# Optimization experiments

Hardware: AMD Instinct MI355X
Metric: run time of the kernel (lower is better)

The kernel has to match this reference:

```python
import jax, jax.numpy as jnp
import numpy as np

N_NODES = 500_000
N_Q = 500_000
H = 8       # heads
MH = 8      # m // heads


def setup_inputs() -> dict:
    key = jax.random.key(0)
    ks = jax.random.split(key, 6)
    q_phi = jax.random.normal(ks[0], (N_Q, H, MH), dtype=jnp.float32)
    phi_k_pos = jax.random.normal(ks[1], (H, MH, N_NODES), dtype=jnp.float32)
    phi_k_neg = jax.random.normal(ks[2], (H, MH, N_NODES), dtype=jnp.float32)
    # degrees are nonnegative counts accumulated in build(); simulate with scaled uniforms
    deg_pos = jax.random.uniform(ks[3], (N_NODES, H), dtype=jnp.float32) * 32.0
    deg_neg = jax.random.uniform(ks[4], (N_NODES, H), dtype=jnp.float32) * 32.0
    k_indices = jax.random.randint(ks[5], (N_Q,), 0, N_NODES)
    return {
        "q_phi": q_phi,
        "phi_k_pos": phi_k_pos,
        "phi_k_neg": phi_k_neg,
        "deg_pos": deg_pos,
        "deg_neg": deg_neg,
        "k_indices": k_indices,
    }


def reference(q_phi, phi_k_pos, phi_k_neg, deg_pos, deg_neg, k_indices):
    # gather cached per-node random-feature sums: [h, mh, Nq] -> [Nq, h, mh]
    pk_pos = jnp.transpose(phi_k_pos[:, :, k_indices], (2, 0, 1))
    pk_neg = jnp.transpose(phi_k_neg[:, :, k_indices], (2, 0, 1))
    # per-head dot product over the feature chunk
    num_pos = jnp.sum(q_phi * pk_pos, axis=-1)  # [Nq, h]
    num_neg = jnp.sum(q_phi * pk_neg, axis=-1)  # [Nq, h]
    # degree-normalize with clamp_min(1)
    den_pos = jnp.maximum(deg_pos[k_indices], 1.0)  # [Nq, h]
    den_neg = jnp.maximum(deg_neg[k_indices], 1.0)
    return (num_pos / den_pos, num_neg / den_neg)
```

## Files before the change

kernel.cpp:

```cpp
#include <hip/hip_runtime.h>
#include <hip/hip_bf16.h>

constexpr int N_NODES = 500000;
constexpr int N_Q     = 500000;
constexpr int H       = 8;
constexpr int FEAT    = 64;
constexpr int TILES   = (N_NODES + 63) / 64;

__global__ __launch_bounds__(256) void transpose_pk(
    const float* __restrict__ pk_pos,
    const float* __restrict__ pk_neg,
    float* __restrict__ dst)
{
    __shared__ float lds[64 * 65];
    const int t  = threadIdx.x;
    const int n0 = blockIdx.x * 64;
    const float* src = blockIdx.y ? pk_neg : pk_pos;
    float* d = dst + (size_t)blockIdx.y * (size_t)N_NODES * FEAT;

    const int nrem = N_NODES - n0;

    {
        const int n4 = (t & 15) * 4;
        const int fb = t >> 4;
        for (int it = 0; it < 4; ++it) {
            const int f = fb + it * 16;
            float4 v = make_float4(0.f, 0.f, 0.f, 0.f);
            const float* s = src + (size_t)f * N_NODES + n0 + n4;
            if (n4 + 3 < nrem) {
                v = *(const float4*)s;
            } else if (n4 < nrem) {
                v.x = s[0];
                if (n4 + 1 < nrem) v.y = s[1];
                if (n4 + 2 < nrem) v.z = s[2];
            }
            float* l = &lds[f * 65 + n4];
            l[0] = v.x; l[1] = v.y; l[2] = v.z; l[3] = v.w;
        }
    }
    __syncthreads();

    {
        const int f4 = (t & 15) * 4;
        const int nb = t >> 4;
        for (int it = 0; it < 4; ++it) {
            const int n = nb + it * 16;
            if (n < nrem) {
                float4 v;
                v.x = lds[(f4 + 0) * 65 + n];
                v.y = lds[(f4 + 1) * 65 + n];
                v.z = lds[(f4 + 2) * 65 + n];
                v.w = lds[(f4 + 3) * 65 + n];
                *(float4*)(d + (size_t)(n0 + n) * FEAT + f4) = v;
            }
        }
    }
}

__global__ __launch_bounds__(256) void iskde_main2(
    const float* __restrict__ q_phi,
    const float* __restrict__ pk_t,
    const float* __restrict__ deg_pos,
    const float* __restrict__ deg_neg,
    const int*   __restrict__ k_idx,
    float*       __restrict__ out)
{
    const int i = blockIdx.x * 256 + threadIdx.x;
    const int q = i >> 3;
    const int h = i & 7;

    const int j = k_idx[q];

    const float4* qp = (const float4*)(q_phi + (size_t)q * FEAT + h * 8);
    const float4* pp = (const float4*)(pk_t + (size_t)j * FEAT + h * 8);
    const float4* pn = (const float4*)(pk_t + ((size_t)N_NODES + (size_t)j) * FEAT + h * 8);

    const float4 a0 = qp[0], a1 = qp[1];
    const float4 b0 = pp[0], b1 = pp[1];
    const float4 c0 = pn[0], c1 = pn[1];

    float sp = a0.x*b0.x + a0.y*b0.y + a0.z*b0.z + a0.w*b0.w
             + a1.x*b1.x + a1.y*b1.y + a1.z*b1.z + a1.w*b1.w;
    float sn = a0.x*c0.x + a0.y*c0.y + a0.z*c0.z + a0.w*c0.w
             + a1.x*c1.x + a1.y*c1.y + a1.z*c1.z + a1.w*c1.w;

    const float dp = fmaxf(deg_pos[(size_t)j * H + h], 1.0f);
    const float dn = fmaxf(deg_neg[(size_t)j * H + h], 1.0f);

    __builtin_nontemporal_store(sp / dp, &out[i]);
    __builtin_nontemporal_store(sn / dn, &out[(size_t)N_Q * H + i]);
}

__global__ __launch_bounds__(256, 4) void iskde_gather_kernel(
    const float* __restrict__ q_phi,
    const float* __restrict__ pk_pos,
    const float* __restrict__ pk_neg,
    const float* __restrict__ deg_pos,
    const float* __restrict__ deg_neg,
    const int*   __restrict__ k_idx,
    float*       __restrict__ out)
{
    const int wave_in_blk = threadIdx.x >> 6;
    const int lane        = threadIdx.x & 63;
    const int q           = blockIdx.x * 4 + wave_in_blk;
    if (q >= N_Q) return;

    const int j = k_idx[q];
    const float qv = q_phi[(size_t)q * FEAT + lane];
    const size_t col = (size_t)lane * (size_t)N_NODES + (size_t)j;
    const float pv = pk_pos[col];
    const float nv = pk_neg[col];

    float sp = qv * pv;
    float sn = qv * nv;
    sp += __shfl_xor(sp, 1, 64);
    sn += __shfl_xor(sn, 1, 64);
    sp += __shfl_xor(sp, 2, 64);
    sn += __shfl_xor(sn, 2, 64);
    sp += __shfl_xor(sp, 4, 64);
    sn += __shfl_xor(sn, 4, 64);

    if ((lane & 7) == 0) {
        const int h = lane >> 3;
        const float dp = fmaxf(deg_pos[(size_t)j * H + h], 1.0f);
        const float dn = fmaxf(deg_neg[(size_t)j * H + h], 1.0f);
        const size_t o = (size_t)q * H + h;
        out[o]                   = sp / dp;
        out[(size_t)N_Q * H + o] = sn / dn;
    }
}

extern "C" void kernel_launch(void* const* d_in, const int* in_sizes, int n_in,
                              void* d_out, int out_size, void* d_ws, size_t ws_size,
                              hipStream_t stream) {
    const float* q_phi   = (const float*)d_in[0];
    const float* pk_pos  = (const float*)d_in[1];
    const float* pk_neg  = (const float*)d_in[2];
    const float* deg_pos = (const float*)d_in[3];
    const float* deg_neg = (const float*)d_in[4];
    const int*   k_idx   = (const int*)d_in[5];
    float*       out     = (float*)d_out;

    const size_t need = (size_t)2 * N_NODES * FEAT * sizeof(float);

    if (ws_size >= need) {
        float* pk_t = (float*)d_ws;
        dim3 tgrid(TILES, 2);
        transpose_pk<<<tgrid, 256, 0, stream>>>(pk_pos, pk_neg, pk_t);

        const int blocks = (N_Q * H) / 256;
        iskde_main2<<<blocks, 256, 0, stream>>>(
            q_phi, pk_t, deg_pos, deg_neg, k_idx, out);
    } else {
        const int blocks = (N_Q + 3) / 4;
        iskde_gather_kernel<<<blocks, 256, 0, stream>>>(
            q_phi, pk_pos, pk_neg, deg_pos, deg_neg, k_idx, out);
    }
}
```

Measured before the change: 452.4 us.

## Bin queries by node tile and compute from LDS-staged feature tiles

Replaces the full transpose of both feature tables into workspace with a counting sort of queries by 64-node bin (histogram, scan, atomic scatter). Each block then loads one 64-node tile of pos/neg features into LDS and answers all queries that map to it. This avoids writing and rereading a 256MB transposed copy. The cost is five small launches, a single-block scan, atomics, and scattered reads of q_phi and output writes in bin order.

```diff
diff --git a/kernel.cpp b/kernel.cpp
--- a/kernel.cpp
+++ b/kernel.cpp
@@ -1,94 +1,159 @@
 #include <hip/hip_runtime.h>
-#include <hip/hip_bf16.h>
 
 constexpr int N_NODES = 500000;
 constexpr int N_Q     = 500000;
 constexpr int H       = 8;
 constexpr int FEAT    = 64;
-constexpr int TILES   = (N_NODES + 63) / 64;
-
-__global__ __launch_bounds__(256) void transpose_pk(
+
+constexpr int TBIN   = 64;
+constexpr int SHIFT  = 6;
+constexpr int NB     = (N_NODES + TBIN - 1) / TBIN;
+constexpr int NB_PAD = 8192;
+constexpr int TP     = TBIN + 1;
+
+__global__ __launch_bounds__(256) void zero_hist(int* __restrict__ hist)
+{
+    const int i = blockIdx.x * 256 + threadIdx.x;
+    if (i < NB_PAD) hist[i] = 0;
+}
+
+__global__ __launch_bounds__(256) void hist_kernel(const int* __restrict__ k_idx,
+                                                   int* __restrict__ hist)
+{
+    int i = blockIdx.x * blockDim.x + threadIdx.x;
+    const int stride = gridDim.x * blockDim.x;
+    for (; i < N_Q; i += stride)
+        atomicAdd(&hist[k_idx[i] >> SHIFT], 1);
+}
+
+__global__ __launch_bounds__(1024) void scan_kernel(const int* __restrict__ hist,
+                                                    int* __restrict__ offsets,
+                                                    int* __restrict__ cursor)
+{
+    __shared__ int sums[1024];
+    const int tid  = threadIdx.x;
+    const int base = tid * 8;
+
+    int loc[8];
+    int run = 0;
+#pragma unroll
+    for (int k = 0; k < 8; ++k) {
+        loc[k] = run;
+        const int idx = base + k;
+        run += (idx < NB) ? hist[idx] : 0;
+    }
+    sums[tid] = run;
+    __syncthreads();
+
+    const int own = run;
+    for (int d = 1; d < 1024; d <<= 1) {
+        const int add = (tid >= d) ? sums[tid - d] : 0;
+        __syncthreads();
+        sums[tid] += add;
+        __syncthreads();
+    }
+    const int excl = sums[tid] - own;
+
+#pragma unroll
+    for (int k = 0; k < 8; ++k) {
+        const int idx = base + k;
+        if (idx <= NB) {
+            const int v = excl + loc[k];
+            offsets[idx] = v;
+            cursor[idx]  = v;
+        }
+    }
+}
+
+__global__ __launch_bounds__(256) void scatter_kernel(const int* __restrict__ k_idx,
+                                                      int* __restrict__ cursor,
+                                                      unsigned* __restrict__ vals)
+{
+    int i = blockIdx.x * blockDim.x + threadIdx.x;
+    const int stride = gridDim.x * blockDim.x;
+    for (; i < N_Q; i += stride) {
+        const int j = k_idx[i];
+        const int b = j >> SHIFT;
+        const int p = atomicAdd(&cursor[b], 1);
+        vals[p] = ((unsigned)i << SHIFT) | (unsigned)(j & (TBIN - 1));
+    }
+}
+
+__global__ __launch_bounds__(256, 4) void iskde_binned(
+    const float* __restrict__ q_phi,
     const float* __restrict__ pk_pos,
     const float* __restrict__ pk_neg,
-    float* __restrict__ dst)
-{
-    __shared__ float lds[64 * 65];
-    const int t  = threadIdx.x;
-    const int n0 = blockIdx.x * 64;
-    const float* src = blockIdx.y ? pk_neg : pk_pos;
-    float* d = dst + (size_t)blockIdx.y * (size_t)N_NODES * FEAT;
-
-    const int nrem = N_NODES - n0;
-
-    {
-        const int n4 = (t & 15) * 4;
-        const int fb = t >> 4;
+    const float* __restrict__ deg_pos,
+    const float* __restrict__ deg_neg,
+    const unsigned* __restrict__ vals,
+    const int* __restrict__ offsets,
+    float* __restrict__ out)
+{
+    __shared__ float lds[2][FEAT][TP];
+
+    const int tid  = threadIdx.x;
+    const int b    = blockIdx.x;
+    const int n0   = b * TBIN;
+    const int nrem = min(TBIN, N_NODES - n0);
+
+#pragma unroll
+    for (int s = 0; s < 2; ++s) {
+        const float* __restrict__ src = s ? pk_neg : pk_pos;
+#pragma unroll
         for (int it = 0; it < 4; ++it) {
-            const int f = fb + it * 16;
+            const int g  = it * 256 + tid;
+            const int f  = g >> 4;
+            const int n4 = (g & 15) * 4;
+            const float* p = src + (size_t)f * N_NODES + n0 + n4;
             float4 v = make_float4(0.f, 0.f, 0.f, 0.f);
-            const float* s = src + (size_t)f * N_NODES + n0 + n4;
             if (n4 + 3 < nrem) {
-                v = *(const float4*)s;
-            } else if (n4 < nrem) {
-                v.x = s[0];
-                if (n4 + 1 < nrem) v.y = s[1];
-                if (n4 + 2 < nrem) v.z = s[2];
+                v = *(const float4*)p;
+            } else {
+                if (n4 + 0 < nrem) v.x = p[0];
+                if (n4 + 1 < nrem) v.y = p[1];
+                if (n4 + 2 < nrem) v.z = p[2];
+                if (n4 + 3 < nrem) v.w = p[3];
             }
-            float* l = &lds[f * 65 + n4];
+            float* l = &lds[s][f][n4];
             l[0] = v.x; l[1] = v.y; l[2] = v.z; l[3] = v.w;
         }
     }
     __syncthreads();
 
-    {
-        const int f4 = (t & 15) * 4;
-        const int nb = t >> 4;
-        for (int it = 0; it < 4; ++it) {
-            const int n = nb + it * 16;
-            if (n < nrem) {
-                float4 v;
-                v.x = lds[(f4 + 0) * 65 + n];
-                v.y = lds[(f4 + 1) * 65 + n];
-                v.z = lds[(f4 + 2) * 65 + n];
-                v.w = lds[(f4 + 3) * 65 + n];
-                *(float4*)(d + (size_t)(n0 + n) * FEAT + f4) = v;
-            }
+    const int start = offsets[b];
+    const int count = offsets[b + 1] - start;
+    const int h    = tid & 7;
+    const int slot = tid >> 3;
+
+    for (int it0 = 0; it0 < count; it0 += 32) {
+        const int qi    = it0 + slot;
+        const bool valid = qi < count;
+        unsigned v = 0;
+        if (valid) v = vals[start + qi];
+        const int q  = (int)(v >> SHIFT);
+        const int dj = (int)(v & (TBIN - 1));
+
+        const float4* qp = (const float4*)(q_phi + (size_t)q * FEAT + h * 8);
+        const float4 a0 = qp[0];
+        const float4 a1 = qp[1];
+
+        const float* lp = &lds[0][h * 8][dj];
+        const float* ln = &lds[1][h * 8][dj];
+        float sp = a0.x * lp[0]      + a0.y * lp[TP]     + a0.z * lp[2 * TP] + a0.w * lp[3 * TP]
+                 + a1.x * lp[4 * TP] + a1.y * lp[5 * TP] + a1.z * lp[6 * TP] + a1.w * lp[7 * TP];
+        float sn = a0.x * ln[0]      + a0.y * ln[TP]     + a0.z * ln[2 * TP] + a0.w * ln[3 * TP]
+                 + a1.x * ln[4 * TP] + a1.y * ln[5 * TP] + a1.z * ln[6 * TP] + a1.w * ln[7 * TP];
+
+        const int j = n0 + dj;
+        const float dp = fmaxf(deg_pos[(size_t)j * H + h], 1.0f);
+        const float dn = fmaxf(deg_neg[(size_t)j * H + h], 1.0f);
+
+        if (valid) {
+            const size_t o = (size_t)q * H + h;
+            __builtin_nontemporal_store(sp / dp, &out[o]);
+            __builtin_nontemporal_store(sn / dn, &out[(size_t)N_Q * H + o]);
         }
     }
-}
-
-__global__ __launch_bounds__(256) void iskde_main2(
-    const float* __restrict__ q_phi,
-    const float* __restrict__ pk_t,
-    const float* __restrict__ deg_pos,
-    const float* __restrict__ deg_neg,
-    const int*   __restrict__ k_idx,
-    float*       __restrict__ out)
-{
-    const int i = blockIdx.x * 256 + threadIdx.x;
-    const int q = i >> 3;
-    const int h = i & 7;
-
-    const int j = k_idx[q];
-
-    const float4* qp = (const float4*)(q_phi + (size_t)q * FEAT + h * 8);
-    const float4* pp = (const float4*)(pk_t + (size_t)j * FEAT + h * 8);
-    const float4* pn = (const float4*)(pk_t + ((size_t)N_NODES + (size_t)j) * FEAT + h * 8);
-
-    const float4 a0 = qp[0], a1 = qp[1];
-    const float4 b0 = pp[0], b1 = pp[1];
-    const float4 c0 = pn[0], c1 = pn[1];
-
-    float sp = a0.x*b0.x + a0.y*b0.y + a0.z*b0.z + a0.w*b0.w
-             + a1.x*b1.x + a1.y*b1.y + a1.z*b1.z + a1.w*b1.w;
-    float sn = a0.x*c0.x + a0.y*c0.y + a0.z*c0.z + a0.w*c0.w
-             + a1.x*c1.x + a1.y*c1.y + a1.z*c1.z + a1.w*c1.w;
-
-    const float dp = fmaxf(deg_pos[(size_t)j * H + h], 1.0f);
-    const float dn = fmaxf(deg_neg[(size_t)j * H + h], 1.0f);
-
-    __builtin_nontemporal_store(sp / dp, &out[i]);
-    __builtin_nontemporal_store(sn / dn, &out[(size_t)N_Q * H + i]);
 }
 
 __global__ __launch_bounds__(256, 4) void iskde_gather_kernel(
@@ -141,16 +206,20 @@
     const int*   k_idx   = (const int*)d_in[5];
     float*       out     = (float*)d_out;
 
-    const size_t need = (size_t)2 * N_NODES * FEAT * sizeof(float);
+    const size_t need = ((size_t)NB_PAD * 3 + 16 + (size_t)N_Q) * sizeof(int);
 
     if (ws_size >= need) {
-        float* pk_t = (float*)d_ws;
-        dim3 tgrid(TILES, 2);
-        transpose_pk<<<tgrid, 256, 0, stream>>>(pk_pos, pk_neg, pk_t);
-
-        const int blocks = (N_Q * H) / 256;
-        iskde_main2<<<blocks, 256, 0, stream>>>(
-            q_phi, pk_t, deg_pos, deg_neg, k_idx, out);
+        int*      hist    = (int*)d_ws;
+        int*      offsets = hist + NB_PAD;
+        int*      cursor  = offsets + NB_PAD + 8;
+        unsigned* vals    = (unsigned*)(cursor + NB_PAD + 8);
+
+        zero_hist<<<(NB_PAD + 255) / 256, 256, 0, stream>>>(hist);
+        hist_kernel<<<1024, 256, 0, stream>>>(k_idx, hist);
+        scan_kernel<<<1, 1024, 0, stream>>>(hist, offsets, cursor);
+        scatter_kernel<<<1024, 256, 0, stream>>>(k_idx, cursor, vals);
+        iskde_binned<<<NB, 256, 0, stream>>>(
+            q_phi, pk_pos, pk_neg, deg_pos, deg_neg, vals, offsets, out);
     } else {
         const int blocks = (N_Q + 3) / 4;
         iskde_gather_kernel<<<blocks, 256, 0, stream>>>(
```

Measured after the change: 469.7 us. 1.04x slower.
